# Performance work log

Measured on AMD Instinct MI355X. Metric: run time of the kernel, lower is better.

The kernel has to match this reference:

```python
import jax, jax.numpy as jnp
import numpy as np

DIM_Q = 512
DIM_K = 512
DIM_V = 512
NUM_HEADS = 8
B, NQ, NK = 4, 2048, 2048


def _linear_init(key, d_in, d_out):
    kw, kb = jax.random.split(key)
    bound = 1.0 / np.sqrt(d_in)
    W = jax.random.uniform(kw, (d_in, d_out), minval=-bound, maxval=bound, dtype=jnp.float32)
    b = jax.random.uniform(kb, (d_out,), minval=-bound, maxval=bound, dtype=jnp.float32)
    return W, b


def setup_inputs() -> dict:
    key = jax.random.key(0)
    ks = jax.random.split(key, 6)
    Q = jax.random.normal(ks[0], (B, NQ, DIM_Q), dtype=jnp.float32)
    K = jax.random.normal(ks[1], (B, NK, DIM_K), dtype=jnp.float32)
    Wq, bq = _linear_init(ks[2], DIM_Q, DIM_V)
    Wk, bk = _linear_init(ks[3], DIM_K, DIM_V)
    Wv, bv = _linear_init(ks[4], DIM_K, DIM_V)
    Wo, bo = _linear_init(ks[5], DIM_V, DIM_V)
    ln0_g = jnp.ones((DIM_V,), jnp.float32)
    ln0_b = jnp.zeros((DIM_V,), jnp.float32)
    ln1_g = jnp.ones((DIM_V,), jnp.float32)
    ln1_b = jnp.zeros((DIM_V,), jnp.float32)
    return {"Q": Q, "K": K, "Wq": Wq, "bq": bq, "Wk": Wk, "bk": bk,
            "Wv": Wv, "bv": bv, "Wo": Wo, "bo": bo,
            "ln0_g": ln0_g, "ln0_b": ln0_b, "ln1_g": ln1_g, "ln1_b": ln1_b}


def _layer_norm(x, g, b, eps=1e-5):
    mu = jnp.mean(x, axis=-1, keepdims=True)
    var = jnp.mean(jnp.square(x - mu), axis=-1, keepdims=True)
    return (x - mu) * jax.lax.rsqrt(var + eps) * g + b


def reference(Q, K, Wq, bq, Wk, bk, Wv, bv, Wo, bo, ln0_g, ln0_b, ln1_g, ln1_b):
    h = NUM_HEADS
    dh = DIM_V // h
    q = Q @ Wq + bq                      # [B, NQ, DIM_V]
    k = K @ Wk + bk                      # [B, NK, DIM_V]
    v = K @ Wv + bv                      # [B, NK, DIM_V]
    qh = q.reshape(B, NQ, h, dh)
    kh = k.reshape(B, NK, h, dh)
    vh = v.reshape(B, NK, h, dh)
    # NOTE: faithful to original — scale by sqrt(dim_V), not sqrt(head_dim)
    scores = jnp.einsum('bqhd,bkhd->bhqk', qh, kh) / jnp.sqrt(jnp.float32(DIM_V))
    A = jax.nn.softmax(scores, axis=-1)  # [B, h, NQ, NK]
    o = jnp.einsum('bhqk,bkhd->bqhd', A, vh) + qh
    H = o.reshape(B, NQ, DIM_V)          # residual with projected Q
    H = _layer_norm(H, ln0_g, ln0_b)
    H = H + jax.nn.relu(H @ Wo + bo)
    H = _layer_norm(H, ln1_g, ln1_b)
    return H
```

## Files before the change

### kernel.cpp

```cpp
#include <hip/hip_runtime.h>

typedef float f32x4 __attribute__((ext_vector_type(4)));
typedef float f32x16 __attribute__((ext_vector_type(16)));
typedef __bf16 bf16x8 __attribute__((ext_vector_type(8)));
typedef unsigned short u16;
typedef unsigned int u32;
typedef u16 u16x8 __attribute__((ext_vector_type(8)));
typedef u16 u16x4 __attribute__((ext_vector_type(4)));
typedef u32 u32x4 __attribute__((ext_vector_type(4)));

#define SCALE2F (0.044194173824159216f * 1.4426950408889634f)
#define UNSCALE (1.0f / SCALE2F)

__device__ __forceinline__ u16 f2bf(float x){ return __builtin_bit_cast(u16, (__bf16)x); }
__device__ __forceinline__ float bf2f(u16 h){ unsigned u = ((unsigned)h) << 16; return __builtin_bit_cast(float, u); }
__device__ __forceinline__ int swz(int r, int byteInRow){ return (r*128 + byteInRow) ^ ((r & 7) << 4); }
__device__ __forceinline__ void gload16(const void* g, void* l) {
  __builtin_amdgcn_global_load_lds(
      (const __attribute__((address_space(1))) void*)g,
      (__attribute__((address_space(3))) void*)l, 16, 0, 0);
}
__device__ __forceinline__ u32 cvtpk(float lo, float hi_) {
  u32 r;
  asm("v_cvt_pk_bf16_f32 %0, %1, %2" : "=v"(r) : "v"(lo), "v"(hi_));
  return r;
}
__device__ __forceinline__ void swap32(u32 &a, u32 &b) {
  asm("v_permlane32_swap_b32 %0, %1" : "+v"(a), "+v"(b));
}

#define MFMA(a,b,c)   __builtin_amdgcn_mfma_f32_16x16x32_bf16((a),(b),(c),0,0,0)
#define MFMA32(a,b,c) __builtin_amdgcn_mfma_f32_32x32x16_bf16((a),(b),(c),0,0,0)

__global__ __launch_bounds__(256) void wprep_k(
    const float* __restrict__ W0, const float* __restrict__ W1,
    const float* __restrict__ W2, const float* __restrict__ W3,
    u16* __restrict__ wt)
{
  __shared__ float tile[64][68];
  const float* Ws[4] = {W0, W1, W2, W3};
  const float* W = Ws[blockIdx.z];
  const float sc = (blockIdx.z == 0) ? SCALE2F : 1.0f;
  u16* out = wt + (size_t)blockIdx.z * 512 * 512;
  int k0 = blockIdx.x * 64, n0 = blockIdx.y * 64;
  int t = threadIdx.x;
  #pragma unroll
  for (int i = 0; i < 2; ++i) {
    int c = t + i*256; int r = c >> 3, k8 = c & 7;
    const float* src = W + (size_t)(k0 + r)*512 + n0 + k8*8;
    *(f32x4*)&tile[r][k8*8]     = *(const f32x4*)src;
    *(f32x4*)&tile[r][k8*8 + 4] = *(const f32x4*)(src + 4);
  }
  __syncthreads();
  #pragma unroll
  for (int i = 0; i < 2; ++i) {
    int c = t + i*256; int r = c >> 3, k8 = c & 7;
    u16x8 h;
    #pragma unroll
    for (int j = 0; j < 8; ++j) h[j] = f2bf(tile[k8*8 + j][r] * sc);
    *(u16x8*)(out + (size_t)(n0 + r)*512 + k0 + k8*8) = h;
  }
}

__global__ __launch_bounds__(512) void proj2_k(
    const float* __restrict__ Qin, const float* __restrict__ Kin,
    const u16* __restrict__ wt,
    const float* __restrict__ bq, const float* __restrict__ bk, const float* __restrict__ bv,
    u16* __restrict__ qbuf, u16* __restrict__ kbuf, u16* __restrict__ vt)
{
  __shared__ __align__(16) u16 lA[2][64*64];
  __shared__ __align__(16) u16 lB0[2][128*64];
  __shared__ __align__(16) u16 lB1[2][128*64];
  int j = blockIdx.x;
  int xcd = j & 7, s = j >> 3;
  int py = s & 3;
  int z  = (s >> 2) & 1;
  int px = (s >> 3) * 8 + xcd;
  const float* A     = z ? Kin : Qin;
  const u16*   Bt0   = wt + (size_t)(z ? 1 : 0) * 262144;
  const u16*   Bt1   = wt + (size_t)2 * 262144;
  const float* bias0 = z ? bk : bq;
  const float bscale = z ? 1.0f : SCALE2F;
  int row0 = px * 64, col0 = py * 128;
  int t = threadIdx.x, lane = t & 63, wid = t >> 6;
  int wr = wid >> 2, wc = wid & 3;
  int l15 = lane & 15, lg = lane >> 4;
  int ar = t >> 3, ak8 = t & 7;
  int br = t >> 3;
  int bsrc = ((t & 7) ^ (br & 7)) << 3;
  const float* Arow = A + (size_t)row0 * 512;
  const u16*   B0row = Bt0 + (size_t)col0 * 512;
  const u16*   B1row = Bt1 + (size_t)col0 * 512;

  f32x4 acc0[2][2] = {}, acc1[2][2] = {};

  #pragma unroll
  for (int i = 0; i < 2; ++i)
    gload16(B0row + (size_t)(br + i*64)*512 + bsrc, (char*)lB0[0] + i*8192 + t*16);
  if (z) {
    #pragma unroll
    for (int i = 0; i < 2; ++i)
      gload16(B1row + (size_t)(br + i*64)*512 + bsrc, (char*)lB1[0] + i*8192 + t*16);
  }
  {
    const float* src = Arow + (size_t)ar*512 + ak8*8;
    f32x4 x0 = *(const f32x4*)src;
    f32x4 x1 = *(const f32x4*)(src + 4);
    u16x8 h;
    #pragma unroll
    for (int jj = 0; jj < 4; ++jj) { h[jj] = f2bf(x0[jj]); h[jj+4] = f2bf(x1[jj]); }
    *(u16x8*)((char*)lA[0] + swz(ar, ak8*16)) = h;
  }
  __syncthreads();

  int cur = 0;
  for (int k0 = 0; k0 < 512; k0 += 64) {
    bool pf = (k0 + 64 < 512);
    f32x4 px0, px1;
    if (pf) {
      #pragma unroll
      for (int i = 0; i < 2; ++i)
        gload16(B0row + (size_t)(br + i*64)*512 + k0 + 64 + bsrc, (char*)lB0[cur^1] + i*8192 + t*16);
      if (z) {
        #pragma unroll
        for (int i = 0; i < 2; ++i)
          gload16(B1row + (size_t)(br + i*64)*512 + k0 + 64 + bsrc, (char*)lB1[cur^1] + i*8192 + t*16);
      }
      const float* src = Arow + (size_t)ar*512 + k0 + 64 + ak8*8;
      px0 = *(const f32x4*)src;
      px1 = *(const f32x4*)(src + 4);
    }
    const char* lAc = (const char*)lA[cur];
    const char* lB0c = (const char*)lB0[cur];
    const char* lB1c = (const char*)lB1[cur];
    #pragma unroll
    for (int ks = 0; ks < 2; ++ks) {
      bf16x8 af[2], b0f[2], b1f[2];
      #pragma unroll
      for (int m = 0; m < 2; ++m)
        af[m] = *(const bf16x8*)(lAc + swz(wr*32 + m*16 + l15, ks*64 + lg*16));
      #pragma unroll
      for (int n = 0; n < 2; ++n) {
        int rb = wc*32 + n*16 + l15;
        b0f[n] = *(const bf16x8*)(lB0c + swz(rb, ks*64 + lg*16));
        if (z) b1f[n] = *(const bf16x8*)(lB1c + swz(rb, ks*64 + lg*16));
      }
      #pragma unroll
      for (int m = 0; m < 2; ++m)
        #pragma unroll
        for (int n = 0; n < 2; ++n) {
          acc0[m][n] = MFMA(af[m], b0f[n], acc0[m][n]);
          if (z) acc1[m][n] = MFMA(af[m], b1f[n], acc1[m][n]);
        }
    }
    if (pf) {
      u16x8 h;
      #pragma unroll
      for (int jj = 0; jj < 4; ++jj) { h[jj] = f2bf(px0[jj]); h[jj+4] = f2bf(px1[jj]); }
      *(u16x8*)((char*)lA[cur^1] + swz(ar, ak8*16)) = h;
    }
    __syncthreads();
    cur ^= 1;
  }

  u16* out0 = z ? kbuf : qbuf;
  #pragma unroll
  for (int m = 0; m < 2; ++m) {
    int rowg = row0 + wr*32 + m*16 + lg*4;
    #pragma unroll
    for (int n = 0; n < 2; ++n) {
      int colg = col0 + wc*32 + n*16 + l15;
      float bvv = bias0[colg] * bscale;
      #pragma unroll
      for (int r = 0; r < 4; ++r)
        out0[(size_t)(rowg + r)*512 + colg] = f2bf(acc0[m][n][r] + bvv);
    }
  }
  if (z) {
    #pragma unroll
    for (int m = 0; m < 2; ++m) {
      int rowg = row0 + wr*32 + m*16 + lg*4;
      int b = rowg >> 11, ntok = rowg & 2047;
      #pragma unroll
      for (int n = 0; n < 2; ++n) {
        int colg = col0 + wc*32 + n*16 + l15;
        float bvv = bv[colg];
        u16x4 hv;
        #pragma unroll
        for (int r = 0; r < 4; ++r) hv[r] = f2bf(acc1[m][n][r] + bvv);
        *(u16x4*)(vt + ((size_t)b*512 + colg)*2048 + ntok) = hv;
      }
    }
  }
}

__device__ __forceinline__ void mk_pb(const f32x16& s, float& ps, bf16x8& f0, bf16x8& f1) {
  float p[16];
  #pragma unroll
  for (int r = 0; r < 16; ++r) p[r] = __builtin_amdgcn_exp2f(s[r]);
  float t0 = (p[0] + p[1])  + (p[2] + p[3]);
  float t1 = (p[4] + p[5])  + (p[6] + p[7]);
  float t2 = (p[8] + p[9])  + (p[10] + p[11]);
  float t3 = (p[12] + p[13]) + (p[14] + p[15]);
  ps += (t0 + t1) + (t2 + t3);
  u32 a0 = cvtpk(p[0],  p[1]),  b0 = cvtpk(p[4],  p[5]);
  u32 a1 = cvtpk(p[2],  p[3]),  b1 = cvtpk(p[6],  p[7]);
  swap32(a0, b0); swap32(a1, b1);
  u32 a2 = cvtpk(p[8],  p[9]),  b2 = cvtpk(p[12], p[13]);
  u32 a3 = cvtpk(p[10], p[11]), b3 = cvtpk(p[14], p[15]);
  swap32(a2, b2); swap32(a3, b3);
  u32x4 w0 = {a0, a1, b0, b1};
  u32x4 w1 = {a2, a3, b2, b3};
  f0 = __builtin_bit_cast(bf16x8, w0);
  f1 = __builtin_bit_cast(bf16x8, w1);
}

__global__ __launch_bounds__(512, 4) void attn_k(
    const u16* __restrict__ qb, const u16* __restrict__ kb,
    const u16* __restrict__ vt, u16* __restrict__ ob)
{
  __shared__ __align__(16) char smem[65536];

  int t = threadIdx.x, lane = t & 63, wid = t >> 6;
  int j = blockIdx.x;
  int xcd = j & 7, slot = j >> 3;
  int qx = slot & 15;
  int bh = ((slot >> 4) << 3) | xcd;
  int b = bh >> 3, h = bh & 7;
  int half = wid >> 2;
  int qw = wid & 3;
  int q0 = qx * 128 + qw * 32;
  int l31 = lane & 31, hi = lane >> 5;

  const u16* kbase = kb + ((size_t)b*2048)*512 + h*64;
  const u16* vbase = vt + ((size_t)b*512 + h*64)*2048;

  int sr = t >> 3;
  int ssrc = ((t & 7) ^ (sr & 7)) << 3;

#define LKB(hf, bf) (smem + ((hf)*2 + (bf))*8192)
#define LVB(hf, bf) (smem + 32768 + ((hf)*2 + (bf))*8192)
#define STAGE(buf, off)                                                           \
  gload16(kbase + (size_t)((off) + sr)*512 + ssrc,        LKB(0,buf) + t*16);     \
  gload16(kbase + (size_t)((off) + 1024 + sr)*512 + ssrc, LKB(1,buf) + t*16);     \
  gload16(vbase + (size_t)sr*2048 + (off) + ssrc,         LVB(0,buf) + t*16);     \
  gload16(vbase + (size_t)sr*2048 + (off) + 1024 + ssrc,  LVB(1,buf) + t*16);

  bf16x8 aq[4];
  {
    const u16* qp = qb + ((size_t)(b*2048 + q0 + l31))*512 + h*64 + hi*8;
    #pragma unroll
    for (int ks = 0; ks < 4; ++ks) aq[ks] = *(const bf16x8*)(qp + ks*16);
  }

  f32x16 acc[2] = {};
  float ps = 0.0f;

  STAGE(0, 0);
  __syncthreads();

  int cur = 0;
  for (int i = 0; i < 16; ++i) {
    if (i + 1 < 16) { STAGE(cur^1, (i+1)*64); }
    const char* lKc = LKB(half, cur);
    const char* lVc = LVB(half, cur);
    bf16x8 pb[4];
    #pragma unroll
    for (int n = 0; n < 2; ++n) {
      f32x16 s = {};
      #pragma unroll
      for (int ks = 0; ks < 4; ++ks) {
        bf16x8 kf = *(const bf16x8*)(lKc + swz(n*32 + l31, ks*32 + hi*16));
        s = MFMA32(kf, aq[ks], s);
      }
      mk_pb(s, ps, pb[2*n], pb[2*n+1]);
    }
    #pragma unroll
    for (int m = 0; m < 2; ++m)
      #pragma unroll
      for (int ks = 0; ks < 4; ++ks) {
        bf16x8 vf = *(const bf16x8*)(lVc + swz(m*32 + l31, ks*32 + hi*16));
        acc[m] = MFMA32(vf, pb[ks], acc[m]);
      }
    __syncthreads();
    cur ^= 1;
  }
#undef STAGE

  ps += __shfl_xor(ps, 32, 64);
  float* cb = (float*)smem;
  if (half == 1) {
    float* dst = cb + qw * 2208;
    #pragma unroll
    for (int m = 0; m < 2; ++m)
      #pragma unroll
      for (int rq = 0; rq < 4; ++rq) {
        f32x4 v = {acc[m][rq*4], acc[m][rq*4+1], acc[m][rq*4+2], acc[m][rq*4+3]};
        *(f32x4*)(dst + l31*68 + m*32 + rq*8 + hi*4) = v;
      }
    if (hi == 0) dst[2176 + l31] = ps;
  }
  __syncthreads();
  if (half == 0) {
    const float* src = cb + qw * 2208;
    float inv = 1.0f / (ps + src[2176 + l31]);
    u16* obase = ob + ((size_t)(b*2048 + q0 + l31))*512 + h*64;
    const u16* qrb = qb + ((size_t)(b*2048 + q0 + l31))*512 + h*64;
    #pragma unroll
    for (int m = 0; m < 2; ++m)
      #pragma unroll
      for (int rq = 0; rq < 4; ++rq) {
        f32x4 other = *(const f32x4*)(src + l31*68 + m*32 + rq*8 + hi*4);
        u16x4 qr4 = *(const u16x4*)(qrb + m*32 + rq*8 + hi*4);
        u16x4 o4;
        #pragma unroll
        for (int e = 0; e < 4; ++e)
          o4[e] = f2bf((acc[m][rq*4 + e] + other[e])*inv + bf2f(qr4[e])*UNSCALE);
        *(u16x4*)(obase + m*32 + rq*8 + hi*4) = o4;
      }
  }
}

__global__ __launch_bounds__(512) void tail_k(
    const u16* __restrict__ ob, const u16* __restrict__ Bt,
    const float* __restrict__ bo,
    const float* __restrict__ g0, const float* __restrict__ b0,
    const float* __restrict__ g1, const float* __restrict__ b1,
    float* __restrict__ out)
{
  __shared__ __align__(16) u16 lA[2][32*64];
  __shared__ __align__(16) u16 lB[2][512*64];
  __shared__ float mu0[32], rs0[32], mu1[32], rs1[32];
  __shared__ float ps1[32][8], ss1[32][8];

  int row0 = blockIdx.x * 32;
  int t = threadIdx.x, lane = t & 63, wid = t >> 6;
  int l15 = lane & 15, lg = lane >> 4;

  {
    int r = t >> 4, c0 = (t & 15) * 32;
    const u16* xp = ob + (size_t)(row0 + r)*512 + c0;
    float s = 0.0f, ss = 0.0f;
    #pragma unroll
    for (int j = 0; j < 4; ++j) {
      u16x8 v = *(const u16x8*)(xp + j*8);
      #pragma unroll
      for (int e = 0; e < 8; ++e) { float f = bf2f(v[e]); s += f; ss += f*f; }
    }
    #pragma unroll
    for (int m = 1; m < 16; m <<= 1) { s += __shfl_xor(s, m, 64); ss += __shfl_xor(ss, m, 64); }
    if ((t & 15) == 0) {
      float mu = s * (1.0f/512.0f);
      float var = ss * (1.0f/512.0f) - mu*mu;
      mu0[r] = mu; rs0[r] = rsqrtf(var + 1e-5f);
    }
  }
  __syncthreads();

  int ar = t >> 3, ak8 = t & 7;
  int br = t >> 3;
  int bsrc = ((t & 7) ^ (br & 7)) << 3;

  auto stageA = [&](int buf, int k0) {
    if (t < 256) {
      u16x8 x = *(const u16x8*)(ob + (size_t)(row0 + ar)*512 + k0 + ak8*8);
      f32x4 gv0 = *(const f32x4*)(g0 + k0 + ak8*8);
      f32x4 gv1 = *(const f32x4*)(g0 + k0 + ak8*8 + 4);
      f32x4 bv0 = *(const f32x4*)(b0 + k0 + ak8*8);
      f32x4 bv1 = *(const f32x4*)(b0 + k0 + ak8*8 + 4);
      float mu = mu0[ar], rs = rs0[ar];
      u16x8 h;
      #pragma unroll
      for (int j = 0; j < 4; ++j) {
        h[j]   = f2bf((bf2f(x[j])   - mu)*rs*gv0[j] + bv0[j]);
        h[j+4] = f2bf((bf2f(x[j+4]) - mu)*rs*gv1[j] + bv1[j]);
      }
      *(u16x8*)((char*)lA[buf] + swz(ar, ak8*16)) = h;
    }
  };

  #pragma unroll
  for (int i = 0; i < 8; ++i)
    gload16(Bt + (size_t)(br + i*64)*512 + bsrc, (char*)lB[0] + i*8192 + t*16);
  stageA(0, 0);
  __syncthreads();

  f32x4 acc[2][4] = {};
  int cur = 0;
  for (int k0 = 0; k0 < 512; k0 += 64) {
    if (k0 + 64 < 512) {
      #pragma unroll
      for (int i = 0; i < 8; ++i)
        gload16(Bt + (size_t)(br + i*64)*512 + k0 + 64 + bsrc, (char*)lB[cur^1] + i*8192 + t*16);
      stageA(cur^1, k0 + 64);
    }
    const char* lAc = (const char*)lA[cur];
    const char* lBc = (const char*)lB[cur];
    #pragma unroll
    for (int ks = 0; ks < 2; ++ks) {
      bf16x8 af[2], bfv[4];
      #pragma unroll
      for (int m = 0; m < 2; ++m)
        af[m] = *(const bf16x8*)(lAc + swz(m*16 + l15, ks*64 + lg*16));
      #pragma unroll
      for (int n = 0; n < 4; ++n)
        bfv[n] = *(const bf16x8*)(lBc + swz(wid*64 + n*16 + l15, ks*64 + lg*16));
      #pragma unroll
      for (int m = 0; m < 2; ++m)
        #pragma unroll
        for (int n = 0; n < 4; ++n)
          acc[m][n] = MFMA(af[m], bfv[n], acc[m][n]);
    }
    __syncthreads();
    cur ^= 1;
  }

  float Gv[2][4][4];
  float sp[2][4] = {}, ssp[2][4] = {};
  #pragma unroll
  for (int n = 0; n < 4; ++n) {
    int colg = wid*64 + n*16 + l15;
    float bov = bo[colg];
    float g0c = g0[colg], b0c = b0[colg];
    #pragma unroll
    for (int m = 0; m < 2; ++m) {
      #pragma unroll
      for (int rr = 0; rr < 4; ++rr) {
        int rit = m*16 + lg*4 + rr;
        float H = (bf2f(ob[(size_t)(row0 + rit)*512 + colg]) - mu0[rit])*rs0[rit]*g0c + b0c;
        float G = H + fmaxf(acc[m][n][rr] + bov, 0.0f);
        Gv[m][n][rr] = G;
        sp[m][rr] += G;
        ssp[m][rr] += G*G;
      }
    }
  }
  #pragma unroll
  for (int msk = 1; msk < 16; msk <<= 1)
    #pragma unroll
    for (int m = 0; m < 2; ++m)
      #pragma unroll
      for (int rr = 0; rr < 4; ++rr) {
        sp[m][rr]  += __shfl_xor(sp[m][rr],  msk, 64);
        ssp[m][rr] += __shfl_xor(ssp[m][rr], msk, 64);
      }
  if (l15 == 0) {
    #pragma unroll
    for (int m = 0; m < 2; ++m)
      #pragma unroll
      for (int rr = 0; rr < 4; ++rr) {
        int rit = m*16 + lg*4 + rr;
        ps1[rit][wid] = sp[m][rr];
        ss1[rit][wid] = ssp[m][rr];
      }
  }
  __syncthreads();
  if (t < 32) {
    float s = 0.0f, ss = 0.0f;
    #pragma unroll
    for (int w = 0; w < 8; ++w) { s += ps1[t][w]; ss += ss1[t][w]; }
    float mu = s * (1.0f/512.0f);
    float var = ss * (1.0f/512.0f) - mu*mu;
    mu1[t] = mu; rs1[t] = rsqrtf(var + 1e-5f);
  }
  __syncthreads();
  #pragma unroll
  for (int n = 0; n < 4; ++n) {
    int colg = wid*64 + n*16 + l15;
    float g1c = g1[colg], b1c = b1[colg];
    #pragma unroll
    for (int m = 0; m < 2; ++m)
      #pragma unroll
      for (int rr = 0; rr < 4; ++rr) {
        int rit = m*16 + lg*4 + rr;
        out[(size_t)(row0 + rit)*512 + colg] =
            (Gv[m][n][rr] - mu1[rit])*rs1[rit]*g1c + b1c;
      }
  }
}

extern "C" void kernel_launch(void* const* d_in, const int* in_sizes, int n_in,
                              void* d_out, int out_size, void* d_ws, size_t ws_size,
                              hipStream_t stream)
{
  const float* Q   = (const float*)d_in[0];
  const float* K   = (const float*)d_in[1];
  const float* Wq  = (const float*)d_in[2];
  const float* bq  = (const float*)d_in[3];
  const float* Wk  = (const float*)d_in[4];
  const float* bk  = (const float*)d_in[5];
  const float* Wv  = (const float*)d_in[6];
  const float* bv  = (const float*)d_in[7];
  const float* Wo  = (const float*)d_in[8];
  const float* bo  = (const float*)d_in[9];
  const float* g0  = (const float*)d_in[10];
  const float* b0  = (const float*)d_in[11];
  const float* g1  = (const float*)d_in[12];
  const float* b1  = (const float*)d_in[13];

  char* ws = (char*)d_ws;
  u16*   wt    = (u16*)(ws + 0);
  u16*   qbuf  = (u16*)(ws + (2u<<20));
  u16*   kbuf  = (u16*)(ws + (10u<<20));
  u16*   vt    = (u16*)(ws + (18u<<20));
  u16*   ob    = (u16*)(ws + (26u<<20));

  wprep_k<<<dim3(8, 8, 4), 256, 0, stream>>>(Wq, Wk, Wv, Wo, wt);
  proj2_k<<<1024, 512, 0, stream>>>(Q, K, wt, bq, bk, bv, qbuf, kbuf, vt);
  attn_k<<<512, 512, 0, stream>>>(qbuf, kbuf, vt, ob);
  tail_k<<<256, 512, 0, stream>>>(ob, wt + 3*262144, bo, g0, b0, g1, b1, (float*)d_out);
}
```

Measured before the change: 94.71 us.

## Enlarge attention blocks to 1024 threads with 4-way key split and dual query tiles

The attention kernel now uses 1024-thread blocks. Each block covers 256 queries, and each wave handles two 32-query tiles, so every K/V fragment loaded from LDS feeds two MFMAs. Keys are split four ways across wave groups instead of two, and partial accumulators are combined through LDS in bf16 rather than fp32. The exp/pack routine is reordered to reduce live registers. The changes aim to raise LDS-fragment reuse and cut K/V staging traffic per query. In exchange the kernel launches only 256 blocks (one wave of blocks at best), register pressure per wave is higher, and the bf16 partial sums lose some precision.

```diff
diff --git a/kernel.cpp b/kernel.cpp
--- a/kernel.cpp
+++ b/kernel.cpp
@@ -195,130 +195,192 @@
 }
 
 __device__ __forceinline__ void mk_pb(const f32x16& s, float& ps, bf16x8& f0, bf16x8& f1) {
-  float p[16];
-  #pragma unroll
-  for (int r = 0; r < 16; ++r) p[r] = __builtin_amdgcn_exp2f(s[r]);
-  float t0 = (p[0] + p[1])  + (p[2] + p[3]);
-  float t1 = (p[4] + p[5])  + (p[6] + p[7]);
-  float t2 = (p[8] + p[9])  + (p[10] + p[11]);
-  float t3 = (p[12] + p[13]) + (p[14] + p[15]);
-  ps += (t0 + t1) + (t2 + t3);
-  u32 a0 = cvtpk(p[0],  p[1]),  b0 = cvtpk(p[4],  p[5]);
-  u32 a1 = cvtpk(p[2],  p[3]),  b1 = cvtpk(p[6],  p[7]);
+  u32 a0, a1, b0, b1;
+  float t0, t1;
+  {
+    float e0 = __builtin_amdgcn_exp2f(s[0]), e1 = __builtin_amdgcn_exp2f(s[1]);
+    float e2 = __builtin_amdgcn_exp2f(s[2]), e3 = __builtin_amdgcn_exp2f(s[3]);
+    a0 = cvtpk(e0, e1); a1 = cvtpk(e2, e3);
+    t0 = (e0 + e1) + (e2 + e3);
+  }
+  {
+    float e0 = __builtin_amdgcn_exp2f(s[4]), e1 = __builtin_amdgcn_exp2f(s[5]);
+    float e2 = __builtin_amdgcn_exp2f(s[6]), e3 = __builtin_amdgcn_exp2f(s[7]);
+    b0 = cvtpk(e0, e1); b1 = cvtpk(e2, e3);
+    t0 += (e0 + e1) + (e2 + e3);
+  }
   swap32(a0, b0); swap32(a1, b1);
-  u32 a2 = cvtpk(p[8],  p[9]),  b2 = cvtpk(p[12], p[13]);
-  u32 a3 = cvtpk(p[10], p[11]), b3 = cvtpk(p[14], p[15]);
+  u32x4 w0 = {a0, a1, b0, b1};
+  f0 = __builtin_bit_cast(bf16x8, w0);
+  u32 a2, a3, b2, b3;
+  {
+    float e0 = __builtin_amdgcn_exp2f(s[8]), e1 = __builtin_amdgcn_exp2f(s[9]);
+    float e2 = __builtin_amdgcn_exp2f(s[10]), e3 = __builtin_amdgcn_exp2f(s[11]);
+    a2 = cvtpk(e0, e1); a3 = cvtpk(e2, e3);
+    t1 = (e0 + e1) + (e2 + e3);
+  }
+  {
+    float e0 = __builtin_amdgcn_exp2f(s[12]), e1 = __builtin_amdgcn_exp2f(s[13]);
+    float e2 = __builtin_amdgcn_exp2f(s[14]), e3 = __builtin_amdgcn_exp2f(s[15]);
+    b2 = cvtpk(e0, e1); b3 = cvtpk(e2, e3);
+    t1 += (e0 + e1) + (e2 + e3);
+  }
   swap32(a2, b2); swap32(a3, b3);
-  u32x4 w0 = {a0, a1, b0, b1};
   u32x4 w1 = {a2, a3, b2, b3};
-  f0 = __builtin_bit_cast(bf16x8, w0);
   f1 = __builtin_bit_cast(bf16x8, w1);
-}
-
-__global__ __launch_bounds__(512, 4) void attn_k(
+  ps += t0 + t1;
+}
+
+__global__ __launch_bounds__(1024, 4) void attn_k(
     const u16* __restrict__ qb, const u16* __restrict__ kb,
     const u16* __restrict__ vt, u16* __restrict__ ob)
 {
-  __shared__ __align__(16) char smem[65536];
+  __shared__ __align__(16) char smem[131072];
 
   int t = threadIdx.x, lane = t & 63, wid = t >> 6;
   int j = blockIdx.x;
-  int xcd = j & 7, slot = j >> 3;
-  int qx = slot & 15;
-  int bh = ((slot >> 4) << 3) | xcd;
+  int xcd = j & 7, s = j >> 3;
+  int qx = s & 7;
+  int bh = ((s >> 3) << 3) | xcd;
   int b = bh >> 3, h = bh & 7;
-  int half = wid >> 2;
-  int qw = wid & 3;
-  int q0 = qx * 128 + qw * 32;
+  int qw = wid & 3, qtr = wid >> 2;
+  int q0 = qx * 256 + qw * 64;
   int l31 = lane & 31, hi = lane >> 5;
 
   const u16* kbase = kb + ((size_t)b*2048)*512 + h*64;
   const u16* vbase = vt + ((size_t)b*512 + h*64)*2048;
 
-  int sr = t >> 3;
-  int ssrc = ((t & 7) ^ (sr & 7)) << 3;
-
-#define LKB(hf, bf) (smem + ((hf)*2 + (bf))*8192)
-#define LVB(hf, bf) (smem + 32768 + ((hf)*2 + (bf))*8192)
-#define STAGE(buf, off)                                                           \
-  gload16(kbase + (size_t)((off) + sr)*512 + ssrc,        LKB(0,buf) + t*16);     \
-  gload16(kbase + (size_t)((off) + 1024 + sr)*512 + ssrc, LKB(1,buf) + t*16);     \
-  gload16(vbase + (size_t)sr*2048 + (off) + ssrc,         LVB(0,buf) + t*16);     \
-  gload16(vbase + (size_t)sr*2048 + (off) + 1024 + ssrc,  LVB(1,buf) + t*16);
-
-  bf16x8 aq[4];
-  {
-    const u16* qp = qb + ((size_t)(b*2048 + q0 + l31))*512 + h*64 + hi*8;
-    #pragma unroll
-    for (int ks = 0; ks < 4; ++ks) aq[ks] = *(const bf16x8*)(qp + ks*16);
-  }
-
-  f32x16 acc[2] = {};
-  float ps = 0.0f;
+  int qt2 = t >> 9, tl = t & 511;
+  int sr = tl >> 3;
+  int ssrc = ((tl & 7) ^ (sr & 7)) << 3;
+
+#define LK(q_, b_) (smem + ((q_)*2 + (b_))*8192)
+#define LV(q_, b_) (smem + 65536 + ((q_)*2 + (b_))*8192)
+#define STAGE(buf, off)                                                                      \
+  gload16(kbase + (size_t)(qt2*512 + (off) + sr)*512 + ssrc,      LK(qt2, buf) + tl*16);     \
+  gload16(kbase + (size_t)((2+qt2)*512 + (off) + sr)*512 + ssrc,  LK(2+qt2, buf) + tl*16);   \
+  gload16(vbase + (size_t)sr*2048 + qt2*512 + (off) + ssrc,       LV(qt2, buf) + tl*16);     \
+  gload16(vbase + (size_t)sr*2048 + (2+qt2)*512 + (off) + ssrc,   LV(2+qt2, buf) + tl*16);
+
+  bf16x8 aqA[4], aqB[4];
+  {
+    const u16* qpA = qb + ((size_t)(b*2048 + q0 + l31))*512 + h*64 + hi*8;
+    const u16* qpB = qpA + (size_t)32*512;
+    #pragma unroll
+    for (int ks = 0; ks < 4; ++ks) {
+      aqA[ks] = *(const bf16x8*)(qpA + ks*16);
+      aqB[ks] = *(const bf16x8*)(qpB + ks*16);
+    }
+  }
+
+  f32x16 accA[2] = {}, accB[2] = {};
+  float psA = 0.0f, psB = 0.0f;
 
   STAGE(0, 0);
   __syncthreads();
 
   int cur = 0;
-  for (int i = 0; i < 16; ++i) {
-    if (i + 1 < 16) { STAGE(cur^1, (i+1)*64); }
-    const char* lKc = LKB(half, cur);
-    const char* lVc = LVB(half, cur);
-    bf16x8 pb[4];
+  for (int i = 0; i < 8; ++i) {
+    if (i + 1 < 8) { STAGE(cur^1, (i+1)*64); }
+    const char* lKc = (const char*)LK(qtr, cur);
+    const char* lVc = (const char*)LV(qtr, cur);
+    bf16x8 pbA[4], pbB[4];
     #pragma unroll
     for (int n = 0; n < 2; ++n) {
-      f32x16 s = {};
+      f32x16 s0 = {}, s1 = {};
       #pragma unroll
       for (int ks = 0; ks < 4; ++ks) {
         bf16x8 kf = *(const bf16x8*)(lKc + swz(n*32 + l31, ks*32 + hi*16));
-        s = MFMA32(kf, aq[ks], s);
-      }
-      mk_pb(s, ps, pb[2*n], pb[2*n+1]);
+        s0 = MFMA32(kf, aqA[ks], s0);
+        s1 = MFMA32(kf, aqB[ks], s1);
+      }
+      mk_pb(s0, psA, pbA[2*n], pbA[2*n+1]);
+      mk_pb(s1, psB, pbB[2*n], pbB[2*n+1]);
     }
     #pragma unroll
     for (int m = 0; m < 2; ++m)
       #pragma unroll
       for (int ks = 0; ks < 4; ++ks) {
         bf16x8 vf = *(const bf16x8*)(lVc + swz(m*32 + l31, ks*32 + hi*16));
-        acc[m] = MFMA32(vf, pb[ks], acc[m]);
+        accA[m] = MFMA32(vf, pbA[ks], accA[m]);
+        accB[m] = MFMA32(vf, pbB[ks], accB[m]);
       }
     __syncthreads();
     cur ^= 1;
   }
 #undef STAGE
 
-  ps += __shfl_xor(ps, 32, 64);
-  float* cb = (float*)smem;
-  if (half == 1) {
-    float* dst = cb + qw * 2208;
+  psA += __shfl_xor(psA, 32, 64);
+  psB += __shfl_xor(psB, 32, 64);
+  u16*   cbh = (u16*)smem;
+  float* cps = (float*)(smem + 98304);
+  if (qtr > 0) {
+    int ub = (qw*3 + (qtr-1)) * 4;
+    #pragma unroll
+    for (int m = 0; m < 2; ++m) {
+      u16x8 h0, h1, g0v, g1v;
+      #pragma unroll
+      for (int e = 0; e < 8; ++e) {
+        h0[e]  = f2bf(accA[m][e]);
+        h1[e]  = f2bf(accA[m][8+e]);
+        g0v[e] = f2bf(accB[m][e]);
+        g1v[e] = f2bf(accB[m][8+e]);
+      }
+      *(u16x8*)(cbh + (ub+m)*1024   + lane*16)     = h0;
+      *(u16x8*)(cbh + (ub+m)*1024   + lane*16 + 8) = h1;
+      *(u16x8*)(cbh + (ub+2+m)*1024 + lane*16)     = g0v;
+      *(u16x8*)(cbh + (ub+2+m)*1024 + lane*16 + 8) = g1v;
+    }
+    if (hi == 0) {
+      cps[((qw*3 + (qtr-1))*2 + 0)*32 + l31] = psA;
+      cps[((qw*3 + (qtr-1))*2 + 1)*32 + l31] = psB;
+    }
+  }
+  __syncthreads();
+  if (qtr == 0) {
+    #pragma unroll
+    for (int qq = 0; qq < 3; ++qq) {
+      int ub = (qw*3 + qq) * 4;
+      #pragma unroll
+      for (int m = 0; m < 2; ++m) {
+        u16x8 h0  = *(const u16x8*)(cbh + (ub+m)*1024   + lane*16);
+        u16x8 h1  = *(const u16x8*)(cbh + (ub+m)*1024   + lane*16 + 8);
+        u16x8 g0v = *(const u16x8*)(cbh + (ub+2+m)*1024 + lane*16);
+        u16x8 g1v = *(const u16x8*)(cbh + (ub+2+m)*1024 + lane*16 + 8);
+        #pragma unroll
+        for (int e = 0; e < 8; ++e) {
+          accA[m][e]   += bf2f(h0[e]);
+          accA[m][8+e] += bf2f(h1[e]);
+          accB[m][e]   += bf2f(g0v[e]);
+          accB[m][8+e] += bf2f(g1v[e]);
+        }
+      }
+      psA += cps[((qw*3 + qq)*2 + 0)*32 + l31];
+      psB += cps[((qw*3 + qq)*2 + 1)*32 + l31];
+    }
+    float invA = 1.0f / psA, invB = 1.0f / psB;
+    u16* oA = ob + ((size_t)(b*2048 + q0 + l31))*512 + h*64;
+    u16* oB = oA + (size_t)32*512;
+    const u16* qrA = qb + ((size_t)(b*2048 + q0 + l31))*512 + h*64;
+    const u16* qrB = qrA + (size_t)32*512;
     #pragma unroll
     for (int m = 0; m < 2; ++m)
       #pragma unroll
       for (int rq = 0; rq < 4; ++rq) {
-        f32x4 v = {acc[m][rq*4], acc[m][rq*4+1], acc[m][rq*4+2], acc[m][rq*4+3]};
-        *(f32x4*)(dst + l31*68 + m*32 + rq*8 + hi*4) = v;
-      }
-    if (hi == 0) dst[2176 + l31] = ps;
-  }
-  __syncthreads();
-  if (half == 0) {
-    const float* src = cb + qw * 2208;
-    float inv = 1.0f / (ps + src[2176 + l31]);
-    u16* obase = ob + ((size_t)(b*2048 + q0 + l31))*512 + h*64;
-    const u16* qrb = qb + ((size_t)(b*2048 + q0 + l31))*512 + h*64;
-    #pragma unroll
-    for (int m = 0; m < 2; ++m)
-      #pragma unroll
-      for (int rq = 0; rq < 4; ++rq) {
-        f32x4 other = *(const f32x4*)(src + l31*68 + m*32 + rq*8 + hi*4);
-        u16x4 qr4 = *(const u16x4*)(qrb + m*32 + rq*8 + hi*4);
-        u16x4 o4;
+        u16x4 qa = *(const u16x4*)(qrA + m*32 + rq*8 + hi*4);
+        u16x4 qv = *(const u16x4*)(qrB + m*32 + rq*8 + hi*4);
+        u16x4 o4a, o4b;
         #pragma unroll
-        for (int e = 0; e < 4; ++e)
-          o4[e] = f2bf((acc[m][rq*4 + e] + other[e])*inv + bf2f(qr4[e])*UNSCALE);
-        *(u16x4*)(obase + m*32 + rq*8 + hi*4) = o4;
-      }
-  }
+        for (int e = 0; e < 4; ++e) {
+          o4a[e] = f2bf(accA[m][rq*4 + e]*invA + bf2f(qa[e])*UNSCALE);
+          o4b[e] = f2bf(accB[m][rq*4 + e]*invB + bf2f(qv[e])*UNSCALE);
+        }
+        *(u16x4*)(oA + m*32 + rq*8 + hi*4) = o4a;
+        *(u16x4*)(oB + m*32 + rq*8 + hi*4) = o4b;
+      }
+  }
+#undef LK
+#undef LV
 }
 
 __global__ __launch_bounds__(512) void tail_k(
@@ -507,6 +569,6 @@
 
   wprep_k<<<dim3(8, 8, 4), 256, 0, stream>>>(Wq, Wk, Wv, Wo, wt);
   proj2_k<<<1024, 512, 0, stream>>>(Q, K, wt, bq, bk, bv, qbuf, kbuf, vt);
-  attn_k<<<512, 512, 0, stream>>>(qbuf, kbuf, vt, ob);
+  attn_k<<<256, 1024, 0, stream>>>(qbuf, kbuf, vt, ob);
   tail_k<<<256, 512, 0, stream>>>(ob, wt + 3*262144, bo, g0, b0, g1, b1, (float*)d_out);
 }
```

Result: slower. 289.4 us (+205.6%).
